# Kernel optimization log

Hardware: AMD Instinct MI355X
Metric: run time of the kernel (lower is better)

## Reference

```python
import jax, jax.numpy as jnp
import numpy as np

B, S, D, H = 2, 2048, 1024, 16
HD = D // H

def setup_inputs() -> dict:
    key = jax.random.key(0)
    ks = jax.random.split(key, 9)
    s = 1.0 / np.sqrt(D)
    inp = {"x": jax.random.normal(ks[0], (B, S, D), dtype=jnp.float32)}
    for i, name in enumerate(["q", "k", "v", "o"]):
        inp[f"W_{name}"] = jax.random.uniform(ks[1 + 2 * i], (D, D), dtype=jnp.float32, minval=-s, maxval=s)
        inp[f"b_{name}"] = jax.random.uniform(ks[2 + 2 * i], (D,), dtype=jnp.float32, minval=-s, maxval=s)
    return inp


def reference(x, W_q, b_q, W_k, b_k, W_v, b_v, W_o, b_o):
    # x: [B, S, D]
    def split_heads(t):
        return t.reshape(B, S, H, HD).transpose(0, 2, 1, 3)  # [B, H, S, HD]

    Q = split_heads(x @ W_q + b_q)
    K = split_heads(x @ W_k + b_k)
    V = split_heads(x @ W_v + b_v)

    scale = 1.0 / np.sqrt(HD).astype(np.float32)
    scores = jnp.einsum("bhqd,bhkd->bhqk", Q, K) * scale  # [B, H, S, S]
    weights = jax.nn.softmax(scores, axis=-1)
    attn = jnp.einsum("bhqk,bhkd->bhqd", weights, V)  # [B, H, S, HD]
    attn = attn.transpose(0, 2, 1, 3).reshape(B, S, D)
    return attn @ W_o + b_o
```

## Files before the change

kernel.cpp:

```cpp
#include <hip/hip_runtime.h>
#include <hip/hip_bf16.h>

#define BB 2
#define SS 2048
#define DD 1024
#define HH 16
#define HD 64

typedef __attribute__((ext_vector_type(8))) short bf16x8;
typedef __attribute__((ext_vector_type(4))) float f32x4;

__device__ __forceinline__ unsigned short f2bf(float f) {
  unsigned int u = __float_as_uint(f);
  return (unsigned short)((u + 0x7FFFu + ((u >> 16) & 1u)) >> 16);
}

__device__ __forceinline__ float fast_exp2(float x) {
#if __has_builtin(__builtin_amdgcn_exp2f)
  return __builtin_amdgcn_exp2f(x);
#else
  return __expf(x * 0.6931471805599453f);
#endif
}

__device__ __forceinline__ void async_copy16(const unsigned short* gp, unsigned short* lp) {
  __builtin_amdgcn_global_load_lds(
      (const __attribute__((address_space(1))) unsigned int*)gp,
      (__attribute__((address_space(3))) unsigned int*)lp, 16, 0, 0);
}

__global__ __launch_bounds__(256) void prep_kernel(
    const float* __restrict__ x, unsigned short* __restrict__ xb,
    const float* __restrict__ W0, unsigned short* __restrict__ T0,
    const float* __restrict__ W1, unsigned short* __restrict__ T1,
    const float* __restrict__ W2, unsigned short* __restrict__ T2,
    const float* __restrict__ W3, unsigned short* __restrict__ T3) {
  const int blk = blockIdx.x;
  const int t = threadIdx.x;
  if (blk < 4096) {
    int i = blk * 1024 + t * 4;
    float4 v = *(const float4*)(x + i);
    ushort4 u;
    u.x = f2bf(v.x); u.y = f2bf(v.y); u.z = f2bf(v.z); u.w = f2bf(v.w);
    *(ushort4*)(xb + i) = u;
    return;
  }
  const int j = blk - 4096;
  const int jw = j >> 10;
  const int tb = j & 1023;
  const float* W = jw == 0 ? W0 : (jw == 1 ? W1 : (jw == 2 ? W2 : W3));
  unsigned short* T = jw == 0 ? T0 : (jw == 1 ? T1 : (jw == 2 ? T2 : T3));
  __shared__ float tile[32][33];
  int k0 = (tb & 31) * 32, n0 = (tb >> 5) * 32;
  int c = t & 31, r0 = t >> 5;
#pragma unroll
  for (int i = 0; i < 4; ++i) {
    int r = r0 + i * 8;
    tile[r][c] = W[(size_t)(k0 + r) * DD + n0 + c];
  }
  __syncthreads();
#pragma unroll
  for (int i = 0; i < 4; ++i) {
    int r = r0 + i * 8;
    T[(size_t)(n0 + r) * DD + k0 + c] = f2bf(tile[c][r]);
  }
}

template <int STORE>
__device__ __forceinline__ void gemm_core(
    const unsigned short* __restrict__ A, const unsigned short* __restrict__ BT,
    const float* __restrict__ bias, void* __restrict__ outp, float scale,
    int bm, int bn) {
  const int t = threadIdx.x;
  const int w = t >> 6;
  const int l = t & 63;
  const int wm = (w >> 1) * 64;
  const int wn = (w & 1) * 64;

  __shared__ __align__(16) unsigned short As[128 * 32];
  __shared__ __align__(16) unsigned short Bs[128 * 32];

  f32x4 acc[4][4];
#pragma unroll
  for (int i = 0; i < 4; ++i)
#pragma unroll
    for (int j = 0; j < 4; ++j) acc[i][j] = (f32x4)0.f;

  const int fr = l & 15;
  const int kg = (l >> 4) * 8;

  for (int k0 = 0; k0 < DD; k0 += 32) {
    __syncthreads();
#pragma unroll
    for (int c = 0; c < 2; ++c) {
      int e = (w * 2 + c) * 512 + l * 8;
      int row = e >> 5, kk = e & 31;
      async_copy16(A + (size_t)(bm + row) * DD + k0 + kk, As + (w * 2 + c) * 512);
      async_copy16(BT + (size_t)(bn + row) * DD + k0 + kk, Bs + (w * 2 + c) * 512);
    }
    __syncthreads();

    bf16x8 af[4], bfr[4];
#pragma unroll
    for (int i = 0; i < 4; ++i)
      af[i] = *(const bf16x8*)(As + (wm + i * 16 + fr) * 32 + kg);
#pragma unroll
    for (int j = 0; j < 4; ++j)
      bfr[j] = *(const bf16x8*)(Bs + (wn + j * 16 + fr) * 32 + kg);
#pragma unroll
    for (int i = 0; i < 4; ++i)
#pragma unroll
      for (int j = 0; j < 4; ++j)
        acc[i][j] = __builtin_amdgcn_mfma_f32_16x16x32_bf16(af[i], bfr[j], acc[i][j], 0, 0, 0);
  }

  const int col_l = l & 15;
  const int row_l = (l >> 4) * 4;

  if (STORE == 2) {
    unsigned short* out = (unsigned short*)outp;
    unsigned int* T = (unsigned int*)As;
    const int b_ = bm >> 11;
    const int srow0 = bm & 2047;
#pragma unroll
    for (int p = 0; p < 4; ++p) {
      __syncthreads();
      if ((w & 1) == (p >> 1)) {
        const int jt0 = (p & 1) * 2;
#pragma unroll
        for (int jj = 0; jj < 2; ++jj) {
          int jt = jt0 + jj;
          int n_p = jj * 16 + col_l;
          float bv = bias[bn + p * 32 + n_p];
#pragma unroll
          for (int i = 0; i < 4; ++i) {
            int m0 = wm + i * 16 + row_l;
#pragma unroll
            for (int pr = 0; pr < 2; ++pr) {
              unsigned int val =
                  (unsigned int)f2bf(acc[i][jt][2 * pr] + bv) |
                  ((unsigned int)f2bf(acc[i][jt][2 * pr + 1] + bv) << 16);
              int m = m0 + 2 * pr;
              T[n_p * 64 + (((m >> 1)) ^ ((n_p & 7) << 2))] = val;
            }
          }
        }
      }
      __syncthreads();
#pragma unroll
      for (int c = 0; c < 2; ++c) {
        int q = t + c * 256;
        int n_p = q >> 4, cpos = q & 15;
        uint4 v = *(const uint4*)(T + n_p * 64 + ((cpos * 4) ^ ((n_p & 7) << 2)));
        int n_glob = bn + p * 32 + n_p;
        int h_ = n_glob >> 6, hd_ = n_glob & 63;
        *(uint4*)(out + ((size_t)((b_ * HH + h_) * HD + hd_)) * SS + srow0 + cpos * 8) = v;
      }
    }
    return;
  }

#pragma unroll
  for (int i = 0; i < 4; ++i) {
    int m_base = bm + wm + i * 16 + row_l;
#pragma unroll
    for (int j = 0; j < 4; ++j) {
      int n = bn + wn + j * 16 + col_l;
      float bv = bias[n];
      if (STORE == 0) {
        float* out = (float*)outp;
#pragma unroll
        for (int r = 0; r < 4; ++r)
          out[(size_t)(m_base + r) * DD + n] = acc[i][j][r] + bv;
      } else {
        unsigned short* out = (unsigned short*)outp;
        int h_ = n >> 6, hd_ = n & 63;
#pragma unroll
        for (int r = 0; r < 4; ++r) {
          int m = m_base + r;
          int b_ = m >> 11, s_ = m & 2047;
          out[(((size_t)(b_ * HH + h_) * SS) + s_) * HD + hd_] =
              f2bf((acc[i][j][r] + bv) * scale);
        }
      }
    }
  }
}

__global__ __launch_bounds__(256) void qkv_gemm_mfma(
    const unsigned short* __restrict__ A,
    const unsigned short* __restrict__ WqT, const unsigned short* __restrict__ WkT,
    const unsigned short* __restrict__ WvT,
    const float* __restrict__ bq, const float* __restrict__ bk,
    const float* __restrict__ bv,
    unsigned short* __restrict__ Qo, unsigned short* __restrict__ Ko,
    unsigned short* __restrict__ VTo) {
  const int bm = blockIdx.y * 128;
  const int which = blockIdx.x >> 3;
  const int bn = (blockIdx.x & 7) * 128;
  if (which == 0)
    gemm_core<1>(A, WqT, bq, (void*)Qo, 0.18033688011112042f, bm, bn);
  else if (which == 1)
    gemm_core<1>(A, WkT, bk, (void*)Ko, 1.0f, bm, bn);
  else
    gemm_core<2>(A, WvT, bv, (void*)VTo, 1.0f, bm, bn);
}

__global__ __launch_bounds__(256) void out_gemm_mfma(
    const unsigned short* __restrict__ A, const unsigned short* __restrict__ WoT,
    const float* __restrict__ bo, float* __restrict__ out) {
  gemm_core<0>(A, WoT, bo, (void*)out, 1.0f, blockIdx.y * 128, blockIdx.x * 128);
}

__global__ __launch_bounds__(256) void flash_attn_mfma(
    const unsigned short* __restrict__ Q,
    const unsigned short* __restrict__ K,
    const unsigned short* __restrict__ VT,
    unsigned short* __restrict__ ctx) {
  const int bh = blockIdx.x;
  const int qt = blockIdx.y;
  const int b  = bh >> 4;
  const int h  = bh & 15;
  const int t  = threadIdx.x;
  const int w  = t >> 6;
  const int l  = t & 63;
  const int g  = l >> 4;
  const int ln = l & 15;

  const unsigned short* Qp = Q + ((size_t)bh * SS + (size_t)qt * 128 + w * 32) * HD;
  const unsigned short* Kp = K + (size_t)bh * SS * HD;
  const unsigned short* Vp = VT + (size_t)bh * HD * SS;

  __shared__ __align__(16) unsigned short Ks[2][64 * 64];
  __shared__ __align__(16) unsigned short Vs[2][64 * 64];

  bf16x8 qf[2][2];
#pragma unroll
  for (int nt = 0; nt < 2; ++nt)
#pragma unroll
    for (int kb = 0; kb < 2; ++kb)
      qf[nt][kb] = *(const bf16x8*)(Qp + (nt * 16 + ln) * HD + kb * 32 + g * 8);

  f32x4 o[2][4];
#pragma unroll
  for (int nt = 0; nt < 2; ++nt)
#pragma unroll
    for (int mt = 0; mt < 4; ++mt) o[nt][mt] = (f32x4)0.f;
  float rs[2] = {0.f, 0.f};

  const int s0 = ((2 * g) & 3) * 16 + ln;
  const int s1 = ((2 * g + 1) & 3) * 16 + ln;
  const bool hi = (g >> 1) != 0;

  auto stage = [&](int kt, int half) {
#pragma unroll
    for (int j = 0; j < 2; ++j) {
      int c = (w * 2 + j) * 64 + l;
      int row = c >> 3, cc = c & 7;
      int gcc = cc ^ (row & 7);
      async_copy16(Kp + (size_t)(kt * 64 + row) * HD + gcc * 8,
                   &Ks[half][(w * 2 + j) * 512]);
      async_copy16(Vp + (size_t)row * SS + kt * 64 + gcc * 8,
                   &Vs[half][(w * 2 + j) * 512]);
    }
  };

  stage(0, 0);
  for (int kt = 0; kt < SS / 64; ++kt) {
    const int half = kt & 1;
    __syncthreads();
    if (kt + 1 < SS / 64) stage(kt + 1, half ^ 1);

    f32x4 st[2][4];
#pragma unroll
    for (int nt = 0; nt < 2; ++nt)
#pragma unroll
      for (int mt = 0; mt < 4; ++mt) st[nt][mt] = (f32x4)0.f;
#pragma unroll
    for (int kb = 0; kb < 2; ++kb)
#pragma unroll
      for (int mt = 0; mt < 4; ++mt) {
        int row = mt * 16 + ln;
        bf16x8 ka = *(const bf16x8*)(&Ks[half][row * 64 + (((kb * 4 + g) ^ (row & 7)) * 8)]);
        st[0][mt] = __builtin_amdgcn_mfma_f32_16x16x32_bf16(ka, qf[0][kb], st[0][mt], 0, 0, 0);
        st[1][mt] = __builtin_amdgcn_mfma_f32_16x16x32_bf16(ka, qf[1][kb], st[1][mt], 0, 0, 0);
      }

    unsigned int pu[2][4][2];
#pragma unroll
    for (int nt = 0; nt < 2; ++nt)
#pragma unroll
      for (int mt = 0; mt < 4; ++mt) {
        float p0 = fast_exp2(st[nt][mt][0]);
        float p1 = fast_exp2(st[nt][mt][1]);
        float p2 = fast_exp2(st[nt][mt][2]);
        float p3 = fast_exp2(st[nt][mt][3]);
        pu[nt][mt][0] = __builtin_amdgcn_perm(__float_as_uint(p1), __float_as_uint(p0),
                                              0x07060302u);
        pu[nt][mt][1] = __builtin_amdgcn_perm(__float_as_uint(p3), __float_as_uint(p2),
                                              0x07060302u);
        rs[nt] += (p0 + p1) + (p2 + p3);
      }

#pragma unroll
    for (int kb = 0; kb < 2; ++kb) {
      bf16x8 pbv[2];
#pragma unroll
      for (int nt = 0; nt < 2; ++nt) {
        unsigned int a0 = __shfl((int)pu[nt][2 * kb][0], s0, 64);
        unsigned int b0 = __shfl((int)pu[nt][2 * kb + 1][0], s0, 64);
        unsigned int a1 = __shfl((int)pu[nt][2 * kb][1], s0, 64);
        unsigned int b1 = __shfl((int)pu[nt][2 * kb + 1][1], s0, 64);
        unsigned int a2 = __shfl((int)pu[nt][2 * kb][0], s1, 64);
        unsigned int b2 = __shfl((int)pu[nt][2 * kb + 1][0], s1, 64);
        unsigned int a3 = __shfl((int)pu[nt][2 * kb][1], s1, 64);
        unsigned int b3 = __shfl((int)pu[nt][2 * kb + 1][1], s1, 64);
        union { unsigned int u[4]; bf16x8 v; } pb;
        pb.u[0] = hi ? b0 : a0;
        pb.u[1] = hi ? b1 : a1;
        pb.u[2] = hi ? b2 : a2;
        pb.u[3] = hi ? b3 : a3;
        pbv[nt] = pb.v;
      }
#pragma unroll
      for (int mt = 0; mt < 4; ++mt) {
        int row = mt * 16 + ln;
        bf16x8 va = *(const bf16x8*)(&Vs[half][row * 64 + (((kb * 4 + g) ^ (row & 7)) * 8)]);
        o[0][mt] = __builtin_amdgcn_mfma_f32_16x16x32_bf16(va, pbv[0], o[0][mt], 0, 0, 0);
        o[1][mt] = __builtin_amdgcn_mfma_f32_16x16x32_bf16(va, pbv[1], o[1][mt], 0, 0, 0);
      }
    }
  }

#pragma unroll
  for (int nt = 0; nt < 2; ++nt) {
    float lsum = rs[nt];
    lsum += __shfl_xor(lsum, 16, 64);
    lsum += __shfl_xor(lsum, 32, 64);
    float inv = 1.f / lsum;
    int srow = qt * 128 + w * 32 + nt * 16 + ln;
    unsigned short* cb = ctx + (size_t)(b * SS + srow) * DD + h * HD;
#pragma unroll
    for (int mt = 0; mt < 4; ++mt) {
      ushort4 u4;
      u4.x = f2bf(o[nt][mt][0] * inv);
      u4.y = f2bf(o[nt][mt][1] * inv);
      u4.z = f2bf(o[nt][mt][2] * inv);
      u4.w = f2bf(o[nt][mt][3] * inv);
      *(ushort4*)(cb + mt * 16 + 4 * g) = u4;
    }
  }
}

extern "C" void kernel_launch(void* const* d_in, const int* in_sizes, int n_in,
                              void* d_out, int out_size, void* d_ws, size_t ws_size,
                              hipStream_t stream) {
  const float* x  = (const float*)d_in[0];
  const float* Wq = (const float*)d_in[1];
  const float* bq = (const float*)d_in[2];
  const float* Wk = (const float*)d_in[3];
  const float* bk = (const float*)d_in[4];
  const float* Wv = (const float*)d_in[5];
  const float* bv = (const float*)d_in[6];
  const float* Wo = (const float*)d_in[7];
  const float* bo = (const float*)d_in[8];
  float* out = (float*)d_out;

  const size_t ELEMS = (size_t)BB * SS * DD;
  char* ws = (char*)d_ws;
  unsigned short* xb   = (unsigned short*)ws;  ws += ELEMS * 2;
  unsigned short* WqT  = (unsigned short*)ws;  ws += (size_t)DD * DD * 2;
  unsigned short* WkT  = (unsigned short*)ws;  ws += (size_t)DD * DD * 2;
  unsigned short* WvT  = (unsigned short*)ws;  ws += (size_t)DD * DD * 2;
  unsigned short* WoT  = (unsigned short*)ws;  ws += (size_t)DD * DD * 2;
  unsigned short* Qb   = (unsigned short*)ws;  ws += ELEMS * 2;
  unsigned short* Kb   = (unsigned short*)ws;  ws += ELEMS * 2;
  unsigned short* VbT  = (unsigned short*)ws;  ws += ELEMS * 2;
  unsigned short* ctxb = (unsigned short*)ws;  ws += ELEMS * 2;

  prep_kernel<<<8192, 256, 0, stream>>>(x, xb, Wq, WqT, Wk, WkT, Wv, WvT, Wo, WoT);

  dim3 qkv_grid(3 * DD / 128, BB * SS / 128);
  qkv_gemm_mfma<<<qkv_grid, 256, 0, stream>>>(xb, WqT, WkT, WvT, bq, bk, bv,
                                              Qb, Kb, VbT);

  dim3 attn_grid(BB * HH, SS / 128);
  flash_attn_mfma<<<attn_grid, 256, 0, stream>>>(Qb, Kb, VbT, ctxb);

  dim3 out_grid(DD / 128, BB * SS / 128);
  out_gemm_mfma<<<out_grid, 256, 0, stream>>>(ctxb, WoT, bo, out);
}
```

Before: 222.6 us.

## Split attention over key halves with combine kernel; double GEMM K-step

The flash attention grid gains a third dimension that splits the key sequence in two. Each half writes unnormalized fp32 partial outputs and row sums, and a new combine kernel adds them, normalizes and converts to bf16. This doubles the attention block count from 512 to 1024 to improve occupancy across CUs, at the cost of extra fp32 global traffic and one more launch. Separately, the GEMM core now stages 64 K-columns per iteration instead of 32, halving the barrier count but doubling shared memory use. The split relies on the softmax using a fixed max (exp2 without running max), so partial sums can be added directly.

Result: slower. 230.0 us (+3.4%).

```diff
diff --git a/kernel.cpp b/kernel.cpp
--- a/kernel.cpp
+++ b/kernel.cpp
@@ -77,8 +77,8 @@
   const int wm = (w >> 1) * 64;
   const int wn = (w & 1) * 64;
 
-  __shared__ __align__(16) unsigned short As[128 * 32];
-  __shared__ __align__(16) unsigned short Bs[128 * 32];
+  __shared__ __align__(16) unsigned short As[128 * 64];
+  __shared__ __align__(16) unsigned short Bs[128 * 64];
 
   f32x4 acc[4][4];
 #pragma unroll
@@ -89,29 +89,36 @@
   const int fr = l & 15;
   const int kg = (l >> 4) * 8;
 
-  for (int k0 = 0; k0 < DD; k0 += 32) {
+  for (int k0 = 0; k0 < DD; k0 += 64) {
     __syncthreads();
 #pragma unroll
-    for (int c = 0; c < 2; ++c) {
-      int e = (w * 2 + c) * 512 + l * 8;
-      int row = e >> 5, kk = e & 31;
-      async_copy16(A + (size_t)(bm + row) * DD + k0 + kk, As + (w * 2 + c) * 512);
-      async_copy16(BT + (size_t)(bn + row) * DD + k0 + kk, Bs + (w * 2 + c) * 512);
+    for (int c = 0; c < 4; ++c) {
+      int e = (w * 4 + c) * 512 + l * 8;
+      int kb_s = e >> 12;
+      int rem = e & 4095;
+      int row = rem >> 5, kk = rem & 31;
+      async_copy16(A + (size_t)(bm + row) * DD + k0 + kb_s * 32 + kk,
+                   As + (w * 4 + c) * 512);
+      async_copy16(BT + (size_t)(bn + row) * DD + k0 + kb_s * 32 + kk,
+                   Bs + (w * 4 + c) * 512);
     }
     __syncthreads();
 
-    bf16x8 af[4], bfr[4];
-#pragma unroll
-    for (int i = 0; i < 4; ++i)
-      af[i] = *(const bf16x8*)(As + (wm + i * 16 + fr) * 32 + kg);
-#pragma unroll
-    for (int j = 0; j < 4; ++j)
-      bfr[j] = *(const bf16x8*)(Bs + (wn + j * 16 + fr) * 32 + kg);
-#pragma unroll
-    for (int i = 0; i < 4; ++i)
+#pragma unroll
+    for (int kb = 0; kb < 2; ++kb) {
+      bf16x8 af[4], bfr[4];
+#pragma unroll
+      for (int i = 0; i < 4; ++i)
+        af[i] = *(const bf16x8*)(As + kb * 4096 + (wm + i * 16 + fr) * 32 + kg);
 #pragma unroll
       for (int j = 0; j < 4; ++j)
-        acc[i][j] = __builtin_amdgcn_mfma_f32_16x16x32_bf16(af[i], bfr[j], acc[i][j], 0, 0, 0);
+        bfr[j] = *(const bf16x8*)(Bs + kb * 4096 + (wn + j * 16 + fr) * 32 + kg);
+#pragma unroll
+      for (int i = 0; i < 4; ++i)
+#pragma unroll
+        for (int j = 0; j < 4; ++j)
+          acc[i][j] = __builtin_amdgcn_mfma_f32_16x16x32_bf16(af[i], bfr[j], acc[i][j], 0, 0, 0);
+    }
   }
 
   const int col_l = l & 15;
@@ -216,9 +223,11 @@
     const unsigned short* __restrict__ Q,
     const unsigned short* __restrict__ K,
     const unsigned short* __restrict__ VT,
-    unsigned short* __restrict__ ctx) {
+    float* __restrict__ Opart,
+    float* __restrict__ Lpart) {
   const int bh = blockIdx.x;
   const int qt = blockIdx.y;
+  const int z  = blockIdx.z;
   const int b  = bh >> 4;
   const int h  = bh & 15;
   const int t  = threadIdx.x;
@@ -251,6 +260,8 @@
   const int s0 = ((2 * g) & 3) * 16 + ln;
   const int s1 = ((2 * g + 1) & 3) * 16 + ln;
   const bool hi = (g >> 1) != 0;
+
+  const int kt0 = z * (SS / 128);
 
   auto stage = [&](int kt, int half) {
 #pragma unroll
@@ -265,11 +276,11 @@
     }
   };
 
-  stage(0, 0);
-  for (int kt = 0; kt < SS / 64; ++kt) {
-    const int half = kt & 1;
+  stage(kt0, 0);
+  for (int it = 0; it < SS / 128; ++it) {
+    const int half = it & 1;
     __syncthreads();
-    if (kt + 1 < SS / 64) stage(kt + 1, half ^ 1);
+    if (it + 1 < SS / 128) stage(kt0 + it + 1, half ^ 1);
 
     f32x4 st[2][4];
 #pragma unroll
@@ -332,24 +343,41 @@
     }
   }
 
+  const size_t ELEMS = (size_t)BB * SS * DD;
 #pragma unroll
   for (int nt = 0; nt < 2; ++nt) {
     float lsum = rs[nt];
     lsum += __shfl_xor(lsum, 16, 64);
     lsum += __shfl_xor(lsum, 32, 64);
-    float inv = 1.f / lsum;
     int srow = qt * 128 + w * 32 + nt * 16 + ln;
-    unsigned short* cb = ctx + (size_t)(b * SS + srow) * DD + h * HD;
-#pragma unroll
-    for (int mt = 0; mt < 4; ++mt) {
-      ushort4 u4;
-      u4.x = f2bf(o[nt][mt][0] * inv);
-      u4.y = f2bf(o[nt][mt][1] * inv);
-      u4.z = f2bf(o[nt][mt][2] * inv);
-      u4.w = f2bf(o[nt][mt][3] * inv);
-      *(ushort4*)(cb + mt * 16 + 4 * g) = u4;
-    }
-  }
+    float* ob = Opart + z * ELEMS + ((size_t)(b * SS + srow)) * DD + h * HD;
+#pragma unroll
+    for (int mt = 0; mt < 4; ++mt)
+      *(f32x4*)(ob + mt * 16 + 4 * g) = o[nt][mt];
+    if (g == 0)
+      Lpart[z * (BB * HH * SS) + (b * HH + h) * SS + srow] = lsum;
+  }
+}
+
+__global__ __launch_bounds__(256) void combine_kernel(
+    const float* __restrict__ Opart, const float* __restrict__ Lpart,
+    unsigned short* __restrict__ ctx) {
+  const size_t ELEMS = (size_t)BB * SS * DD;
+  int idx = (blockIdx.x * 256 + threadIdx.x) * 4;
+  float4 a = *(const float4*)(Opart + idx);
+  float4 c = *(const float4*)(Opart + ELEMS + idx);
+  int sg = idx >> 10;
+  int d  = idx & 1023;
+  int b = sg >> 11, s = sg & 2047;
+  int h = d >> 6;
+  int li = (b * HH + h) * SS + s;
+  float inv = 1.f / (Lpart[li] + Lpart[BB * HH * SS + li]);
+  ushort4 u;
+  u.x = f2bf((a.x + c.x) * inv);
+  u.y = f2bf((a.y + c.y) * inv);
+  u.z = f2bf((a.z + c.z) * inv);
+  u.w = f2bf((a.w + c.w) * inv);
+  *(ushort4*)(ctx + idx) = u;
 }
 
 extern "C" void kernel_launch(void* const* d_in, const int* in_sizes, int n_in,
@@ -377,6 +405,8 @@
   unsigned short* Kb   = (unsigned short*)ws;  ws += ELEMS * 2;
   unsigned short* VbT  = (unsigned short*)ws;  ws += ELEMS * 2;
   unsigned short* ctxb = (unsigned short*)ws;  ws += ELEMS * 2;
+  float* Opart = (float*)ws;                   ws += 2 * ELEMS * 4;
+  float* Lpart = (float*)ws;                   ws += 2 * (size_t)BB * HH * SS * 4;
 
   prep_kernel<<<8192, 256, 0, stream>>>(x, xb, Wq, WqT, Wk, WkT, Wv, WvT, Wo, WoT);
 
@@ -384,8 +414,10 @@
   qkv_gemm_mfma<<<qkv_grid, 256, 0, stream>>>(xb, WqT, WkT, WvT, bq, bk, bv,
                                               Qb, Kb, VbT);
 
-  dim3 attn_grid(BB * HH, SS / 128);
-  flash_attn_mfma<<<attn_grid, 256, 0, stream>>>(Qb, Kb, VbT, ctxb);
+  dim3 attn_grid(BB * HH, SS / 128, 2);
+  flash_attn_mfma<<<attn_grid, 256, 0, stream>>>(Qb, Kb, VbT, Opart, Lpart);
+
+  combine_kernel<<<ELEMS / 1024, 256, 0, stream>>>(Opart, Lpart, ctxb);
 
   dim3 out_grid(DD / 128, BB * SS / 128);
   out_gemm_mfma<<<out_grid, 256, 0, stream>>>(ctxb, WoT, bo, out);
```

## Route softmax probabilities through LDS and remap GEMM blocks per XCD

Applied to the files above, without the earlier changes.

In the attention kernel, the bf16 probabilities are now written into a per-wave swizzled LDS buffer and read back in the layout the PV MFMA expects. This replaces 16 cross-lane shuffles plus selects per k-block. The QKV and output GEMMs switch to 1D grids whose block index is decoded so that consecutive blocks on the same XCD share the same M rows, aiming for better L2 reuse. The cost is 16KB of extra shared memory, which may lower occupancy, and the LDS write-then-read happens with no explicit barrier, relying on wave-local ordering.

Measured after the change: 216.8 us. 1.03x faster.

```diff
diff --git a/kernel.cpp b/kernel.cpp
--- a/kernel.cpp
+++ b/kernel.cpp
@@ -195,9 +195,13 @@
     const float* __restrict__ bv,
     unsigned short* __restrict__ Qo, unsigned short* __restrict__ Ko,
     unsigned short* __restrict__ VTo) {
-  const int bm = blockIdx.y * 128;
-  const int which = blockIdx.x >> 3;
-  const int bn = (blockIdx.x & 7) * 128;
+  const int i = blockIdx.x;
+  const int xcd = i & 7;
+  const int slot = i >> 3;
+  const int bm = (xcd + 8 * (slot / 24)) * 128;
+  const int c = slot % 24;
+  const int which = c >> 3;
+  const int bn = (c & 7) * 128;
   if (which == 0)
     gemm_core<1>(A, WqT, bq, (void*)Qo, 0.18033688011112042f, bm, bn);
   else if (which == 1)
@@ -209,7 +213,12 @@
 __global__ __launch_bounds__(256) void out_gemm_mfma(
     const unsigned short* __restrict__ A, const unsigned short* __restrict__ WoT,
     const float* __restrict__ bo, float* __restrict__ out) {
-  gemm_core<0>(A, WoT, bo, (void*)out, 1.0f, blockIdx.y * 128, blockIdx.x * 128);
+  const int i = blockIdx.x;
+  const int xcd = i & 7;
+  const int slot = i >> 3;
+  const int bm = (xcd + 8 * (slot >> 3)) * 128;
+  const int bn = (slot & 7) * 128;
+  gemm_core<0>(A, WoT, bo, (void*)out, 1.0f, bm, bn);
 }
 
 __global__ __launch_bounds__(256) void flash_attn_mfma(
@@ -233,6 +242,7 @@
 
   __shared__ __align__(16) unsigned short Ks[2][64 * 64];
   __shared__ __align__(16) unsigned short Vs[2][64 * 64];
+  __shared__ __align__(16) unsigned short Ps[4][32 * 64];
 
   bf16x8 qf[2][2];
 #pragma unroll
@@ -248,9 +258,7 @@
     for (int mt = 0; mt < 4; ++mt) o[nt][mt] = (f32x4)0.f;
   float rs[2] = {0.f, 0.f};
 
-  const int s0 = ((2 * g) & 3) * 16 + ln;
-  const int s1 = ((2 * g + 1) & 3) * 16 + ln;
-  const bool hi = (g >> 1) != 0;
+  char* pw = (char*)&Ps[w][0];
 
   auto stage = [&](int kt, int half) {
 #pragma unroll
@@ -286,41 +294,35 @@
         st[1][mt] = __builtin_amdgcn_mfma_f32_16x16x32_bf16(ka, qf[1][kb], st[1][mt], 0, 0, 0);
       }
 
-    unsigned int pu[2][4][2];
-#pragma unroll
-    for (int nt = 0; nt < 2; ++nt)
+#pragma unroll
+    for (int nt = 0; nt < 2; ++nt) {
+      const int q = nt * 16 + ln;
+      const int qs = q & 7;
 #pragma unroll
       for (int mt = 0; mt < 4; ++mt) {
         float p0 = fast_exp2(st[nt][mt][0]);
         float p1 = fast_exp2(st[nt][mt][1]);
         float p2 = fast_exp2(st[nt][mt][2]);
         float p3 = fast_exp2(st[nt][mt][3]);
-        pu[nt][mt][0] = __builtin_amdgcn_perm(__float_as_uint(p1), __float_as_uint(p0),
-                                              0x07060302u);
-        pu[nt][mt][1] = __builtin_amdgcn_perm(__float_as_uint(p3), __float_as_uint(p2),
-                                              0x07060302u);
+        uint2 v2;
+        v2.x = __builtin_amdgcn_perm(__float_as_uint(p1), __float_as_uint(p0),
+                                     0x07060302u);
+        v2.y = __builtin_amdgcn_perm(__float_as_uint(p3), __float_as_uint(p2),
+                                     0x07060302u);
         rs[nt] += (p0 + p1) + (p2 + p3);
-      }
+        int chunk = (2 * mt + (g >> 1)) ^ qs;
+        *(uint2*)(pw + q * 128 + chunk * 16 + (g & 1) * 8) = v2;
+      }
+    }
 
 #pragma unroll
     for (int kb = 0; kb < 2; ++kb) {
       bf16x8 pbv[2];
 #pragma unroll
       for (int nt = 0; nt < 2; ++nt) {
-        unsigned int a0 = __shfl((int)pu[nt][2 * kb][0], s0, 64);
-        unsigned int b0 = __shfl((int)pu[nt][2 * kb + 1][0], s0, 64);
-        unsigned int a1 = __shfl((int)pu[nt][2 * kb][1], s0, 64);
-        unsigned int b1 = __shfl((int)pu[nt][2 * kb + 1][1], s0, 64);
-        unsigned int a2 = __shfl((int)pu[nt][2 * kb][0], s1, 64);
-        unsigned int b2 = __shfl((int)pu[nt][2 * kb + 1][0], s1, 64);
-        unsigned int a3 = __shfl((int)pu[nt][2 * kb][1], s1, 64);
-        unsigned int b3 = __shfl((int)pu[nt][2 * kb + 1][1], s1, 64);
-        union { unsigned int u[4]; bf16x8 v; } pb;
-        pb.u[0] = hi ? b0 : a0;
-        pb.u[1] = hi ? b1 : a1;
-        pb.u[2] = hi ? b2 : a2;
-        pb.u[3] = hi ? b3 : a3;
-        pbv[nt] = pb.v;
+        const int q = nt * 16 + ln;
+        int chunk = (4 * kb + g) ^ (q & 7);
+        pbv[nt] = *(const bf16x8*)(pw + q * 128 + chunk * 16);
       }
 #pragma unroll
       for (int mt = 0; mt < 4; ++mt) {
@@ -380,13 +382,11 @@
 
   prep_kernel<<<8192, 256, 0, stream>>>(x, xb, Wq, WqT, Wk, WkT, Wv, WvT, Wo, WoT);
 
-  dim3 qkv_grid(3 * DD / 128, BB * SS / 128);
-  qkv_gemm_mfma<<<qkv_grid, 256, 0, stream>>>(xb, WqT, WkT, WvT, bq, bk, bv,
-                                              Qb, Kb, VbT);
+  qkv_gemm_mfma<<<768, 256, 0, stream>>>(xb, WqT, WkT, WvT, bq, bk, bv,
+                                         Qb, Kb, VbT);
 
   dim3 attn_grid(BB * HH, SS / 128);
   flash_attn_mfma<<<attn_grid, 256, 0, stream>>>(Qb, Kb, VbT, ctxb);
 
-  dim3 out_grid(DD / 128, BB * SS / 128);
-  out_gemm_mfma<<<out_grid, 256, 0, stream>>>(ctxb, WoT, bo, out);
-}
+  out_gemm_mfma<<<256, 256, 0, stream>>>(ctxb, WoT, bo, out);
+}
```
